# Optimization experiments

Measured on AMD Instinct MI355X. Metric: run time of the kernel, lower is better.

Reference implementation:

```python
import jax, jax.numpy as jnp
import numpy as np
import math

MAX_F, B, D = 512, 32, 1024
H, NUM_OUT = 16, 4
S = D // H  # subspace size = 64
FC_HID = 4096
MASK_VAL = -50.0  # the original writes -50 (not -inf) into padded logits


def setup_inputs() -> dict:
    key = jax.random.key(0)
    k = jax.random.split(key, 7)
    x = jax.random.normal(k[0], (MAX_F, B, D), dtype=jnp.float32)
    num_frames = jax.random.randint(k[1], (B,), 1, MAX_F + 1)
    query = jax.random.normal(k[2], (NUM_OUT, H, S), dtype=jnp.float32)  # attn_query_vecs
    W1 = jax.random.normal(k[3], (D * NUM_OUT, FC_HID), dtype=jnp.float32) * 0.02
    b1 = jnp.zeros((FC_HID,), dtype=jnp.float32)
    W2 = jax.random.normal(k[4], (FC_HID, NUM_OUT), dtype=jnp.float32) * 0.02
    b2 = jnp.zeros((NUM_OUT,), dtype=jnp.float32)
    return {"x": x, "num_frames": num_frames, "query": query,
            "W1": W1, "b1": b1, "W2": W2, "b2": b2}


def reference(x, num_frames, query, W1, b1, W2, b2):
    # x: (F, B, D) padded per-frame features (encoder = identity, pad value irrelevant
    # because we re-mask below, matching pad-with-zeros in the original).
    F, Bz, Dz = x.shape
    O, Hh, Ss = query.shape
    scale = math.sqrt(Ss)
    mask = jnp.arange(F)[:, None] < num_frames[None, :]            # (F, B)
    hq = x.reshape(F, Bz, Hh, Ss)                                  # (F, B, H, S)
    # per-head query-key dot products for all num_out queries at once
    alpha = jnp.einsum('fbhs,ohs->ofbh', hq, query) / scale        # (O, F, B, H)
    alpha = jnp.where(mask[None, :, :, None], alpha, MASK_VAL)
    attn = jax.nn.softmax(alpha, axis=1)                           # softmax over frames
    h_pad = jnp.where(mask[:, :, None, None], hq, 0.0)             # zero-padded features
    h_vid = jnp.einsum('fbhs,ofbh->obhs', h_pad, attn)             # (O, B, H, S)
    # stack(dim=1) then view(B, -1) -> concat num_out feature blocks per sample
    h_cat = jnp.transpose(h_vid, (1, 0, 2, 3)).reshape(Bz, O * Hh * Ss)
    out = jax.nn.relu(h_cat @ W1 + b1) @ W2 + b2                   # (B, num_out)
    return out, attn
```

## Files before the change

kernel.cpp:

```cpp
#include <hip/hip_runtime.h>
#include <math.h>

#define MAXF 512
#define BZ   32
#define DD   1024
#define HH   16
#define OO   4
#define SS   64
#define FCH  4096
#define KPARTS 8

typedef __attribute__((ext_vector_type(8))) short short8;
typedef __attribute__((ext_vector_type(4))) float f32x4;

__device__ inline short f2bf(float f) {
    unsigned u = __float_as_uint(f);
    u += 0x7FFFu + ((u >> 16) & 1u);
    return (short)(u >> 16);
}

__global__ __launch_bounds__(256) void logits_kernel(
    const float* __restrict__ x, const int* __restrict__ num_frames,
    const float* __restrict__ query, float* __restrict__ logits,
    float2* __restrict__ cstats)
{
    __shared__ __align__(16) float tile[64][68];
    __shared__ __align__(16) float sq[OO][64];

    const int tid   = threadIdx.x;
    const int bh    = blockIdx.x >> 3;
    const int fc    = blockIdx.x & 7;
    const int b     = bh >> 4, h = bh & 15;
    const int nf    = num_frames[b];
    const int fbase = fc * 64;
    const bool act  = (fbase < nf);

    const int o = tid >> 6, f = tid & 63;
    sq[o][f] = query[(size_t)(o * HH + h) * SS + f];

    if (act) {
        #pragma unroll
        for (int k = 0; k < 4; ++k) {
            int idx = tid + k * 256;
            int fr = idx >> 4, s4 = (idx & 15) * 4;
            float4 v = *(const float4*)(x + (size_t)(fbase + fr) * (BZ * DD)
                                          + (size_t)b * DD + h * SS + s4);
            *(float4*)&tile[fr][s4] = v;
        }
    }
    __syncthreads();

    float lg = -50.0f;
    if (act) {
        const float4* trow = (const float4*)&tile[f][0];
        const float4* qrow = (const float4*)&sq[o][0];
        float dot = 0.f;
        #pragma unroll
        for (int i = 0; i < 16; ++i) {
            float4 t = trow[i];
            float4 q = qrow[i];
            dot += t.x * q.x + t.y * q.y + t.z * q.z + t.w * q.w;
        }
        if (fbase + f < nf) lg = dot * 0.125f;
    }
    logits[((size_t)bh * OO + o) * MAXF + fbase + f] = lg;

    float mc = lg;
    #pragma unroll
    for (int d = 32; d; d >>= 1) mc = fmaxf(mc, __shfl_xor(mc, d, 64));
    float sc = __expf(lg - mc);
    #pragma unroll
    for (int d = 32; d; d >>= 1) sc += __shfl_xor(sc, d, 64);
    if (f == 0) cstats[(bh * OO + o) * 8 + fc] = make_float2(mc, sc);
}

__global__ __launch_bounds__(256) void wsum_kernel(
    const float* __restrict__ x, const int* __restrict__ num_frames,
    const float* __restrict__ query, const float2* __restrict__ cstats,
    float* __restrict__ hcat)
{
    __shared__ __align__(16) float tile[64][68];
    __shared__ __align__(16) float sq[OO][64];
    __shared__ __align__(16) float attc[OO][64];

    const int tid   = threadIdx.x;
    const int bh    = blockIdx.x >> 3;
    const int fc    = blockIdx.x & 7;
    const int b     = bh >> 4, h = bh & 15;
    const int nf    = num_frames[b];
    const int fbase = fc * 64;
    const bool act  = (fbase < nf);

    if (!act && fc != 0) return;

    const int o = tid >> 6, lane = tid & 63;
    sq[o][lane] = query[(size_t)(o * HH + h) * SS + lane];

    if (act) {
        #pragma unroll
        for (int k = 0; k < 4; ++k) {
            int idx = tid + k * 256;
            int fr = idx >> 4, s4 = (idx & 15) * 4;
            float4 v = *(const float4*)(x + (size_t)(fbase + fr) * (BZ * DD)
                                          + (size_t)b * DD + h * SS + s4);
            *(float4*)&tile[fr][s4] = v;
        }
    }
    __syncthreads();

    const float2* cs = cstats + (bh * OO + o) * 8;
    float m = -1e30f;
    #pragma unroll
    for (int k = 0; k < 8; ++k) m = fmaxf(m, cs[k].x);
    float s = 0.f;
    #pragma unroll
    for (int k = 0; k < 8; ++k) s += cs[k].y * __expf(cs[k].x - m);
    const float inv = 1.0f / s;

    float p = 0.f;
    if (act) {
        const float4* trow = (const float4*)&tile[lane][0];
        const float4* qrow = (const float4*)&sq[o][0];
        float dot = 0.f;
        #pragma unroll
        for (int i = 0; i < 16; ++i) {
            float4 t = trow[i];
            float4 q = qrow[i];
            dot += t.x * q.x + t.y * q.y + t.z * q.z + t.w * q.w;
        }
        if (fbase + lane < nf) p = __expf(dot * 0.125f - m) * inv;
    }
    attc[o][lane] = p;
    __syncthreads();

    float acc = 0.f;
    if (act) {
        const float4* a4 = (const float4*)&attc[o][0];
        #pragma unroll
        for (int i = 0; i < 16; ++i) {
            float4 a = a4[i];
            acc += a.x * tile[i * 4 + 0][lane];
            acc += a.y * tile[i * 4 + 1][lane];
            acc += a.z * tile[i * 4 + 2][lane];
            acc += a.w * tile[i * 4 + 3][lane];
        }
    }
    const float POIS = (fc == 0) ? __uint_as_float(0xAAAAAAAAu) : 0.f;
    atomicAdd(&hcat[(size_t)b * FCH + o * (HH * SS) + h * SS + lane], acc - POIS);
}

__global__ __launch_bounds__(256) void attn_out_kernel(
    const float* __restrict__ logits, const float2* __restrict__ cstats,
    float* __restrict__ attn_out)
{
    __shared__ float tile[64][65];
    __shared__ float sm[64], sv[64];
    const int o     = blockIdx.z;
    const int fbase = blockIdx.x * 64;
    const int gbase = blockIdx.y * 64;
    const int c  = threadIdx.x & 63;
    const int r4 = threadIdx.x >> 6;

    if (threadIdx.x < 64) {
        const float2* cs = cstats + ((gbase + threadIdx.x) * OO + o) * 8;
        float m = -1e30f;
        #pragma unroll
        for (int k = 0; k < 8; ++k) m = fmaxf(m, cs[k].x);
        float s = 0.f;
        #pragma unroll
        for (int k = 0; k < 8; ++k) s += cs[k].y * __expf(cs[k].x - m);
        sm[threadIdx.x] = m;
        sv[threadIdx.x] = 1.0f / s;
    }
    for (int r = r4; r < 64; r += 4)
        tile[r][c] = logits[((size_t)(gbase + r) * OO + o) * MAXF + fbase + c];
    __syncthreads();
    for (int r = r4; r < 64; r += 4)
        attn_out[((size_t)o * MAXF + fbase + r) * (BZ * HH) + gbase + c] =
            __expf(tile[c][r] - sm[c]) * sv[c];
}

__global__ __launch_bounds__(256) void fc1_mfma_kernel(
    const float* __restrict__ hcat, const float* __restrict__ W1,
    float* __restrict__ part)
{
    const int tid  = threadIdx.x;
    const int w    = tid >> 6;
    const int lane = tid & 63;
    const int L15  = lane & 15, q = lane >> 4;
    const int j0   = blockIdx.x * 64 + w * 16;
    const int kp   = blockIdx.y;
    const int k0   = kp * 512;

    f32x4 acc0 = {0.f, 0.f, 0.f, 0.f};
    f32x4 acc1 = {0.f, 0.f, 0.f, 0.f};

    #pragma unroll 2
    for (int s = 0; s < 16; ++s) {
        const int kk = k0 + s * 32 + q * 8;

        const float4* a0p = (const float4*)(hcat + (size_t)L15 * FCH + kk);
        const float4* a1p = (const float4*)(hcat + (size_t)(L15 + 16) * FCH + kk);
        float4 a0l = a0p[0], a0h = a0p[1];
        float4 a1l = a1p[0], a1h = a1p[1];
        short8 af0, af1;
        af0[0]=f2bf(a0l.x); af0[1]=f2bf(a0l.y); af0[2]=f2bf(a0l.z); af0[3]=f2bf(a0l.w);
        af0[4]=f2bf(a0h.x); af0[5]=f2bf(a0h.y); af0[6]=f2bf(a0h.z); af0[7]=f2bf(a0h.w);
        af1[0]=f2bf(a1l.x); af1[1]=f2bf(a1l.y); af1[2]=f2bf(a1l.z); af1[3]=f2bf(a1l.w);
        af1[4]=f2bf(a1h.x); af1[5]=f2bf(a1h.y); af1[6]=f2bf(a1h.z); af1[7]=f2bf(a1h.w);

        const float* bp = W1 + (size_t)kk * FCH + j0 + L15;
        short8 bf;
        bf[0] = f2bf(bp[0 * (size_t)FCH]);
        bf[1] = f2bf(bp[1 * (size_t)FCH]);
        bf[2] = f2bf(bp[2 * (size_t)FCH]);
        bf[3] = f2bf(bp[3 * (size_t)FCH]);
        bf[4] = f2bf(bp[4 * (size_t)FCH]);
        bf[5] = f2bf(bp[5 * (size_t)FCH]);
        bf[6] = f2bf(bp[6 * (size_t)FCH]);
        bf[7] = f2bf(bp[7 * (size_t)FCH]);

        acc0 = __builtin_amdgcn_mfma_f32_16x16x32_bf16(af0, bf, acc0, 0, 0, 0);
        acc1 = __builtin_amdgcn_mfma_f32_16x16x32_bf16(af1, bf, acc1, 0, 0, 0);
    }

    float* pout = part + (size_t)kp * 32 * FCH;
    #pragma unroll
    for (int r = 0; r < 4; ++r) {
        pout[(size_t)(q * 4 + r) * FCH + j0 + L15]        = acc0[r];
        pout[(size_t)(16 + q * 4 + r) * FCH + j0 + L15]   = acc1[r];
    }
}

__global__ __launch_bounds__(256) void fc2_kernel(
    const float* __restrict__ part, const float* __restrict__ b1,
    const float* __restrict__ W2, const float* __restrict__ b2,
    float* __restrict__ out)
{
    __shared__ float red[4][4];
    const int b = blockIdx.x, tid = threadIdx.x;
    float a0 = 0.f, a1 = 0.f, a2 = 0.f, a3 = 0.f;
    #pragma unroll
    for (int k = 0; k < 4; ++k) {
        int j4 = tid + k * 256;
        float4 hv = make_float4(0.f, 0.f, 0.f, 0.f);
        #pragma unroll
        for (int kp = 0; kp < KPARTS; ++kp) {
            float4 pv = ((const float4*)(part + (size_t)(kp * 32 + b) * FCH))[j4];
            hv.x += pv.x; hv.y += pv.y; hv.z += pv.z; hv.w += pv.w;
        }
        float4 bv = ((const float4*)b1)[j4];
        float h0 = fmaxf(hv.x + bv.x, 0.f), h1 = fmaxf(hv.y + bv.y, 0.f);
        float h2 = fmaxf(hv.z + bv.z, 0.f), h3 = fmaxf(hv.w + bv.w, 0.f);
        float4 w0 = ((const float4*)W2)[j4 * 4 + 0];
        float4 w1 = ((const float4*)W2)[j4 * 4 + 1];
        float4 w2 = ((const float4*)W2)[j4 * 4 + 2];
        float4 w3 = ((const float4*)W2)[j4 * 4 + 3];
        a0 += h0 * w0.x + h1 * w1.x + h2 * w2.x + h3 * w3.x;
        a1 += h0 * w0.y + h1 * w1.y + h2 * w2.y + h3 * w3.y;
        a2 += h0 * w0.z + h1 * w1.z + h2 * w2.z + h3 * w3.z;
        a3 += h0 * w0.w + h1 * w1.w + h2 * w2.w + h3 * w3.w;
    }
    #pragma unroll
    for (int d = 32; d; d >>= 1) {
        a0 += __shfl_xor(a0, d, 64);
        a1 += __shfl_xor(a1, d, 64);
        a2 += __shfl_xor(a2, d, 64);
        a3 += __shfl_xor(a3, d, 64);
    }
    const int wv = tid >> 6, lane = tid & 63;
    if (lane == 0) { red[wv][0] = a0; red[wv][1] = a1; red[wv][2] = a2; red[wv][3] = a3; }
    __syncthreads();
    if (tid < 4) {
        float s = red[0][tid] + red[1][tid] + red[2][tid] + red[3][tid] + b2[tid];
        out[b * OO + tid] = s;
    }
}

extern "C" void kernel_launch(void* const* d_in, const int* in_sizes, int n_in,
                              void* d_out, int out_size, void* d_ws, size_t ws_size,
                              hipStream_t stream)
{
    const float* x          = (const float*)d_in[0];
    const int*   num_frames = (const int*)  d_in[1];
    const float* query      = (const float*)d_in[2];
    const float* W1         = (const float*)d_in[3];
    const float* b1         = (const float*)d_in[4];
    const float* W2         = (const float*)d_in[5];
    const float* b2         = (const float*)d_in[6];

    float* out      = (float*)d_out;
    float* attn_out = out + BZ * OO;

    float*  ws        = (float*)d_ws;
    float*  ws_logits = ws;
    float2* ws_cstats = (float2*)(ws + 1048576);
    float*  ws_hcat   = ws + 1048576 + 32768;
    float*  ws_part   = ws_logits;

    logits_kernel  <<<4096, 256, 0, stream>>>(x, num_frames, query, ws_logits, ws_cstats);
    wsum_kernel    <<<4096, 256, 0, stream>>>(x, num_frames, query, ws_cstats, ws_hcat);
    attn_out_kernel<<<dim3(8, 8, 4), 256, 0, stream>>>(ws_logits, ws_cstats, attn_out);
    fc1_mfma_kernel<<<dim3(64, KPARTS), 256, 0, stream>>>(ws_hcat, W1, ws_part);
    fc2_kernel     <<<BZ, 256, 0, stream>>>(ws_part, b1, W2, b2, out);
}
```

Measured before the change: 190.8 us.

## Fuse logits and weighted-sum into single-pass online-softmax attention kernel

```diff
diff --git a/kernel.cpp b/kernel.cpp
--- a/kernel.cpp
+++ b/kernel.cpp
@@ -19,138 +19,188 @@
     return (short)(u >> 16);
 }
 
-__global__ __launch_bounds__(256) void logits_kernel(
+#define MUL4(A,S)  do{ (A).x*=(S); (A).y*=(S); (A).z*=(S); (A).w*=(S); }while(0)
+#define FMA4(A,P,V) do{ (A).x += (P)*(V).x; (A).y += (P)*(V).y; \
+                        (A).z += (P)*(V).z; (A).w += (P)*(V).w; }while(0)
+#define RSUMF(F) do{ F += __shfl_xor(F,4,64); F += __shfl_xor(F,8,64); \
+                     F += __shfl_xor(F,16,64); F += __shfl_xor(F,32,64); }while(0)
+#define RMAXF(F) do{ F = fmaxf(F,__shfl_xor(F,4,64)); F = fmaxf(F,__shfl_xor(F,8,64)); \
+                     F = fmaxf(F,__shfl_xor(F,16,64)); F = fmaxf(F,__shfl_xor(F,32,64)); }while(0)
+#define BFLY4(A) do{ RSUMF((A).x); RSUMF((A).y); RSUMF((A).z); RSUMF((A).w); }while(0)
+#define CCOMP(V,C) ((C)==0?(V).x:(C)==1?(V).y:(C)==2?(V).z:(V).w)
+#define GETJ(V0,V1,V2,V3,J) ((J)<4?CCOMP(V0,(J)&3):(J)<8?CCOMP(V1,(J)&3): \
+                             (J)<12?CCOMP(V2,(J)&3):CCOMP(V3,(J)&3))
+#define DOT16(R,QA,QB,QC,QD) \
+    R = xa0.x*(QA).x + xa0.y*(QA).y + xa0.z*(QA).z + xa0.w*(QA).w \
+      + xa1.x*(QB).x + xa1.y*(QB).y + xa1.z*(QB).z + xa1.w*(QB).w \
+      + xa2.x*(QC).x + xa2.y*(QC).y + xa2.z*(QC).z + xa2.w*(QC).w \
+      + xa3.x*(QD).x + xa3.y*(QD).y + xa3.z*(QD).z + xa3.w*(QD).w
+#define SCALE_ACC() do{ \
+    MUL4(a00,sc0);MUL4(a01,sc0);MUL4(a02,sc0);MUL4(a03,sc0); \
+    MUL4(a10,sc1);MUL4(a11,sc1);MUL4(a12,sc1);MUL4(a13,sc1); \
+    MUL4(a20,sc2);MUL4(a21,sc2);MUL4(a22,sc2);MUL4(a23,sc2); \
+    MUL4(a30,sc3);MUL4(a31,sc3);MUL4(a32,sc3);MUL4(a33,sc3); }while(0)
+
+__global__ __launch_bounds__(256) void attn_fused_kernel(
     const float* __restrict__ x, const int* __restrict__ num_frames,
     const float* __restrict__ query, float* __restrict__ logits,
-    float2* __restrict__ cstats)
-{
-    __shared__ __align__(16) float tile[64][68];
-    __shared__ __align__(16) float sq[OO][64];
-
-    const int tid   = threadIdx.x;
-    const int bh    = blockIdx.x >> 3;
-    const int fc    = blockIdx.x & 7;
-    const int b     = bh >> 4, h = bh & 15;
-    const int nf    = num_frames[b];
-    const int fbase = fc * 64;
-    const bool act  = (fbase < nf);
-
-    const int o = tid >> 6, f = tid & 63;
-    sq[o][f] = query[(size_t)(o * HH + h) * SS + f];
-
-    if (act) {
+    float2* __restrict__ fstats, float* __restrict__ hcat)
+{
+    __shared__ __align__(16) float sq[OO][SS];
+    __shared__ float wmS[4][OO], wsS[4][OO];
+    __shared__ __align__(16) float accsh[4][4][16][OO];
+
+    const int tid  = threadIdx.x;
+    const int bh   = blockIdx.x;
+    const int b    = bh >> 4, h = bh & 15;
+    const int nf   = num_frames[b];
+    const int w    = tid >> 6;
+    const int lane = tid & 63;
+    const int sg   = tid & 3;
+    const int fch  = tid >> 2;
+
+    sq[w][lane] = query[(size_t)(w * HH + h) * SS + lane];
+    __syncthreads();
+
+    float4 q00,q01,q02,q03,q10,q11,q12,q13,q20,q21,q22,q23,q30,q31,q32,q33;
+    {
+        const float4* q0 = (const float4*)&sq[0][0];
+        q00=q0[sg]; q01=q0[sg+4]; q02=q0[sg+8]; q03=q0[sg+12];
+        const float4* q1 = (const float4*)&sq[1][0];
+        q10=q1[sg]; q11=q1[sg+4]; q12=q1[sg+8]; q13=q1[sg+12];
+        const float4* q2 = (const float4*)&sq[2][0];
+        q20=q2[sg]; q21=q2[sg+4]; q22=q2[sg+8]; q23=q2[sg+12];
+        const float4* q3 = (const float4*)&sq[3][0];
+        q30=q3[sg]; q31=q3[sg+4]; q32=q3[sg+8]; q33=q3[sg+12];
+    }
+
+    const float* xbase = x + (size_t)b * DD + (size_t)h * SS;
+
+    float m0=-1e30f,m1=-1e30f,m2=-1e30f,m3=-1e30f;
+    float s0=0.f,s1=0.f,s2=0.f,s3=0.f;
+    float4 a00={0,0,0,0},a01={0,0,0,0},a02={0,0,0,0},a03={0,0,0,0};
+    float4 a10={0,0,0,0},a11={0,0,0,0},a12={0,0,0,0},a13={0,0,0,0};
+    float4 a20={0,0,0,0},a21={0,0,0,0},a22={0,0,0,0},a23={0,0,0,0};
+    float4 a30={0,0,0,0},a31={0,0,0,0},a32={0,0,0,0},a33={0,0,0,0};
+
+    float4 xa0,xa1,xa2,xa3;
+    {
+        const float4* p = (const float4*)(xbase + (size_t)fch * (BZ*DD));
+        xa0=p[sg]; xa1=p[sg+4]; xa2=p[sg+8]; xa3=p[sg+12];
+    }
+
+    #pragma unroll
+    for (int fc = 0; fc < 8; ++fc) {
+        const int fbase = fc * 64;
+        const bool act  = (fbase < nf);
+        float4 xb0={0,0,0,0},xb1={0,0,0,0},xb2={0,0,0,0},xb3={0,0,0,0};
+        const bool actn = (fc < 7) && (fbase + 64 < nf);
+        if (actn) {
+            const float4* p = (const float4*)(xbase + (size_t)(fbase + 64 + fch) * (BZ*DD));
+            xb0=p[sg]; xb1=p[sg+4]; xb2=p[sg+8]; xb3=p[sg+12];
+        }
+        if (act) {
+            float d0,d1,d2,d3;
+            DOT16(d0,q00,q01,q02,q03);
+            DOT16(d1,q10,q11,q12,q13);
+            DOT16(d2,q20,q21,q22,q23);
+            DOT16(d3,q30,q31,q32,q33);
+            d0 += __shfl_xor(d0,1,64); d0 += __shfl_xor(d0,2,64);
+            d1 += __shfl_xor(d1,1,64); d1 += __shfl_xor(d1,2,64);
+            d2 += __shfl_xor(d2,1,64); d2 += __shfl_xor(d2,2,64);
+            d3 += __shfl_xor(d3,1,64); d3 += __shfl_xor(d3,2,64);
+            const bool valid = (fbase + fch) < nf;
+            float lg0 = valid ? d0 * 0.125f : -50.f;
+            float lg1 = valid ? d1 * 0.125f : -50.f;
+            float lg2 = valid ? d2 * 0.125f : -50.f;
+            float lg3 = valid ? d3 * 0.125f : -50.f;
+            float c0=lg0,c1=lg1,c2=lg2,c3=lg3;
+            RMAXF(c0); RMAXF(c1); RMAXF(c2); RMAXF(c3);
+            float n0=fmaxf(m0,c0), n1=fmaxf(m1,c1), n2=fmaxf(m2,c2), n3=fmaxf(m3,c3);
+            float e0=__expf(lg0-n0), e1=__expf(lg1-n1), e2=__expf(lg2-n2), e3=__expf(lg3-n3);
+            float t0=e0,t1=e1,t2=e2,t3=e3;
+            RSUMF(t0); RSUMF(t1); RSUMF(t2); RSUMF(t3);
+            float sc0=__expf(m0-n0), sc1=__expf(m1-n1), sc2=__expf(m2-n2), sc3=__expf(m3-n3);
+            s0 = s0*sc0 + t0; s1 = s1*sc1 + t1; s2 = s2*sc2 + t2; s3 = s3*sc3 + t3;
+            m0=n0; m1=n1; m2=n2; m3=n3;
+            if (sc0<1.f || sc1<1.f || sc2<1.f || sc3<1.f) SCALE_ACC();
+            float p0 = valid ? e0 : 0.f;
+            float p1 = valid ? e1 : 0.f;
+            float p2 = valid ? e2 : 0.f;
+            float p3 = valid ? e3 : 0.f;
+            FMA4(a00,p0,xa0); FMA4(a01,p0,xa1); FMA4(a02,p0,xa2); FMA4(a03,p0,xa3);
+            FMA4(a10,p1,xa0); FMA4(a11,p1,xa1); FMA4(a12,p1,xa2); FMA4(a13,p1,xa3);
+            FMA4(a20,p2,xa0); FMA4(a21,p2,xa1); FMA4(a22,p2,xa2); FMA4(a23,p2,xa3);
+            FMA4(a30,p3,xa0); FMA4(a31,p3,xa1); FMA4(a32,p3,xa2); FMA4(a33,p3,xa3);
+            float lgw = sg==0?lg0 : sg==1?lg1 : sg==2?lg2 : lg3;
+            logits[((size_t)bh*OO + sg)*MAXF + fbase + fch] = lgw;
+        } else {
+            float n0=fmaxf(m0,-50.f), n1=fmaxf(m1,-50.f), n2=fmaxf(m2,-50.f), n3=fmaxf(m3,-50.f);
+            float sc0=__expf(m0-n0), sc1=__expf(m1-n1), sc2=__expf(m2-n2), sc3=__expf(m3-n3);
+            s0 = s0*sc0 + 16.f*__expf(-50.f-n0);
+            s1 = s1*sc1 + 16.f*__expf(-50.f-n1);
+            s2 = s2*sc2 + 16.f*__expf(-50.f-n2);
+            s3 = s3*sc3 + 16.f*__expf(-50.f-n3);
+            if (sc0<1.f || sc1<1.f || sc2<1.f || sc3<1.f) SCALE_ACC();
+            m0=n0; m1=n1; m2=n2; m3=n3;
+            logits[((size_t)bh*OO + sg)*MAXF + fbase + fch] = -50.f;
+        }
+        xa0=xb0; xa1=xb1; xa2=xb2; xa3=xb3;
+    }
+
+    if (lane == 0) {
+        wmS[w][0]=m0; wmS[w][1]=m1; wmS[w][2]=m2; wmS[w][3]=m3;
+        wsS[w][0]=s0; wsS[w][1]=s1; wsS[w][2]=s2; wsS[w][3]=s3;
+    }
+    __syncthreads();
+    float gm0 = fmaxf(fmaxf(wmS[0][0],wmS[1][0]), fmaxf(wmS[2][0],wmS[3][0]));
+    float gm1 = fmaxf(fmaxf(wmS[0][1],wmS[1][1]), fmaxf(wmS[2][1],wmS[3][1]));
+    float gm2 = fmaxf(fmaxf(wmS[0][2],wmS[1][2]), fmaxf(wmS[2][2],wmS[3][2]));
+    float gm3 = fmaxf(fmaxf(wmS[0][3],wmS[1][3]), fmaxf(wmS[2][3],wmS[3][3]));
+    float gs0 = wsS[0][0]*__expf(wmS[0][0]-gm0) + wsS[1][0]*__expf(wmS[1][0]-gm0)
+              + wsS[2][0]*__expf(wmS[2][0]-gm0) + wsS[3][0]*__expf(wmS[3][0]-gm0);
+    float gs1 = wsS[0][1]*__expf(wmS[0][1]-gm1) + wsS[1][1]*__expf(wmS[1][1]-gm1)
+              + wsS[2][1]*__expf(wmS[2][1]-gm1) + wsS[3][1]*__expf(wmS[3][1]-gm1);
+    float gs2 = wsS[0][2]*__expf(wmS[0][2]-gm2) + wsS[1][2]*__expf(wmS[1][2]-gm2)
+              + wsS[2][2]*__expf(wmS[2][2]-gm2) + wsS[3][2]*__expf(wmS[3][2]-gm2);
+    float gs3 = wsS[0][3]*__expf(wmS[0][3]-gm3) + wsS[1][3]*__expf(wmS[1][3]-gm3)
+              + wsS[2][3]*__expf(wmS[2][3]-gm3) + wsS[3][3]*__expf(wmS[3][3]-gm3);
+    float scl0=__expf(m0-gm0), scl1=__expf(m1-gm1), scl2=__expf(m2-gm2), scl3=__expf(m3-gm3);
+
+    BFLY4(a00); BFLY4(a01); BFLY4(a02); BFLY4(a03);
+    BFLY4(a10); BFLY4(a11); BFLY4(a12); BFLY4(a13);
+    BFLY4(a20); BFLY4(a21); BFLY4(a22); BFLY4(a23);
+    BFLY4(a30); BFLY4(a31); BFLY4(a32); BFLY4(a33);
+
+    if ((lane >> 2) == 0) {
         #pragma unroll
-        for (int k = 0; k < 4; ++k) {
-            int idx = tid + k * 256;
-            int fr = idx >> 4, s4 = (idx & 15) * 4;
-            float4 v = *(const float4*)(x + (size_t)(fbase + fr) * (BZ * DD)
-                                          + (size_t)b * DD + h * SS + s4);
-            *(float4*)&tile[fr][s4] = v;
+        for (int j = 0; j < 16; ++j) {
+            float v0 = GETJ(a00,a01,a02,a03,j) * scl0;
+            float v1 = GETJ(a10,a11,a12,a13,j) * scl1;
+            float v2 = GETJ(a20,a21,a22,a23,j) * scl2;
+            float v3 = GETJ(a30,a31,a32,a33,j) * scl3;
+            *(float4*)&accsh[w][sg][j][0] = make_float4(v0,v1,v2,v3);
         }
     }
     __syncthreads();
-
-    float lg = -50.0f;
-    if (act) {
-        const float4* trow = (const float4*)&tile[f][0];
-        const float4* qrow = (const float4*)&sq[o][0];
-        float dot = 0.f;
-        #pragma unroll
-        for (int i = 0; i < 16; ++i) {
-            float4 t = trow[i];
-            float4 q = qrow[i];
-            dot += t.x * q.x + t.y * q.y + t.z * q.z + t.w * q.w;
-        }
-        if (fbase + f < nf) lg = dot * 0.125f;
-    }
-    logits[((size_t)bh * OO + o) * MAXF + fbase + f] = lg;
-
-    float mc = lg;
-    #pragma unroll
-    for (int d = 32; d; d >>= 1) mc = fmaxf(mc, __shfl_xor(mc, d, 64));
-    float sc = __expf(lg - mc);
-    #pragma unroll
-    for (int d = 32; d; d >>= 1) sc += __shfl_xor(sc, d, 64);
-    if (f == 0) cstats[(bh * OO + o) * 8 + fc] = make_float2(mc, sc);
-}
-
-__global__ __launch_bounds__(256) void wsum_kernel(
-    const float* __restrict__ x, const int* __restrict__ num_frames,
-    const float* __restrict__ query, const float2* __restrict__ cstats,
-    float* __restrict__ hcat)
-{
-    __shared__ __align__(16) float tile[64][68];
-    __shared__ __align__(16) float sq[OO][64];
-    __shared__ __align__(16) float attc[OO][64];
-
-    const int tid   = threadIdx.x;
-    const int bh    = blockIdx.x >> 3;
-    const int fc    = blockIdx.x & 7;
-    const int b     = bh >> 4, h = bh & 15;
-    const int nf    = num_frames[b];
-    const int fbase = fc * 64;
-    const bool act  = (fbase < nf);
-
-    if (!act && fc != 0) return;
-
-    const int o = tid >> 6, lane = tid & 63;
-    sq[o][lane] = query[(size_t)(o * HH + h) * SS + lane];
-
-    if (act) {
-        #pragma unroll
-        for (int k = 0; k < 4; ++k) {
-            int idx = tid + k * 256;
-            int fr = idx >> 4, s4 = (idx & 15) * 4;
-            float4 v = *(const float4*)(x + (size_t)(fbase + fr) * (BZ * DD)
-                                          + (size_t)b * DD + h * SS + s4);
-            *(float4*)&tile[fr][s4] = v;
-        }
-    }
-    __syncthreads();
-
-    const float2* cs = cstats + (bh * OO + o) * 8;
-    float m = -1e30f;
-    #pragma unroll
-    for (int k = 0; k < 8; ++k) m = fmaxf(m, cs[k].x);
-    float s = 0.f;
-    #pragma unroll
-    for (int k = 0; k < 8; ++k) s += cs[k].y * __expf(cs[k].x - m);
-    const float inv = 1.0f / s;
-
-    float p = 0.f;
-    if (act) {
-        const float4* trow = (const float4*)&tile[lane][0];
-        const float4* qrow = (const float4*)&sq[o][0];
-        float dot = 0.f;
-        #pragma unroll
-        for (int i = 0; i < 16; ++i) {
-            float4 t = trow[i];
-            float4 q = qrow[i];
-            dot += t.x * q.x + t.y * q.y + t.z * q.z + t.w * q.w;
-        }
-        if (fbase + lane < nf) p = __expf(dot * 0.125f - m) * inv;
-    }
-    attc[o][lane] = p;
-    __syncthreads();
-
-    float acc = 0.f;
-    if (act) {
-        const float4* a4 = (const float4*)&attc[o][0];
-        #pragma unroll
-        for (int i = 0; i < 16; ++i) {
-            float4 a = a4[i];
-            acc += a.x * tile[i * 4 + 0][lane];
-            acc += a.y * tile[i * 4 + 1][lane];
-            acc += a.z * tile[i * 4 + 2][lane];
-            acc += a.w * tile[i * 4 + 3][lane];
-        }
-    }
-    const float POIS = (fc == 0) ? __uint_as_float(0xAAAAAAAAu) : 0.f;
-    atomicAdd(&hcat[(size_t)b * FCH + o * (HH * SS) + h * SS + lane], acc - POIS);
+    {
+        const int oo = tid >> 6, s = tid & 63;
+        const int ssg = (s >> 2) & 3, sj = ((s >> 4) << 2) | (s & 3);
+        float v = accsh[0][ssg][sj][oo] + accsh[1][ssg][sj][oo]
+                + accsh[2][ssg][sj][oo] + accsh[3][ssg][sj][oo];
+        float gso = oo==0?gs0 : oo==1?gs1 : oo==2?gs2 : gs3;
+        hcat[(size_t)b*FCH + (size_t)oo*(HH*SS) + h*SS + s] = v * (1.0f/gso);
+    }
+    if (tid == 0) {
+        fstats[bh*OO+0] = make_float2(gm0, 1.0f/gs0);
+        fstats[bh*OO+1] = make_float2(gm1, 1.0f/gs1);
+        fstats[bh*OO+2] = make_float2(gm2, 1.0f/gs2);
+        fstats[bh*OO+3] = make_float2(gm3, 1.0f/gs3);
+    }
 }
 
 __global__ __launch_bounds__(256) void attn_out_kernel(
-    const float* __restrict__ logits, const float2* __restrict__ cstats,
+    const float* __restrict__ logits, const float2* __restrict__ fstats,
     float* __restrict__ attn_out)
 {
     __shared__ float tile[64][65];
@@ -162,15 +212,9 @@
     const int r4 = threadIdx.x >> 6;
 
     if (threadIdx.x < 64) {
-        const float2* cs = cstats + ((gbase + threadIdx.x) * OO + o) * 8;
-        float m = -1e30f;
-        #pragma unroll
-        for (int k = 0; k < 8; ++k) m = fmaxf(m, cs[k].x);
-        float s = 0.f;
-        #pragma unroll
-        for (int k = 0; k < 8; ++k) s += cs[k].y * __expf(cs[k].x - m);
-        sm[threadIdx.x] = m;
-        sv[threadIdx.x] = 1.0f / s;
+        float2 st = fstats[(gbase + threadIdx.x) * OO + o];
+        sm[threadIdx.x] = st.x;
+        sv[threadIdx.x] = st.y;
     }
     for (int r = r4; r < 64; r += 4)
         tile[r][c] = logits[((size_t)(gbase + r) * OO + o) * MAXF + fbase + c];
@@ -294,13 +338,13 @@
 
     float*  ws        = (float*)d_ws;
     float*  ws_logits = ws;
-    float2* ws_cstats = (float2*)(ws + 1048576);
-    float*  ws_hcat   = ws + 1048576 + 32768;
+    float2* ws_fstats = (float2*)(ws + 1048576);
+    float*  ws_hcat   = ws + 1048576 + 4096;
     float*  ws_part   = ws_logits;
 
-    logits_kernel  <<<4096, 256, 0, stream>>>(x, num_frames, query, ws_logits, ws_cstats);
-    wsum_kernel    <<<4096, 256, 0, stream>>>(x, num_frames, query, ws_cstats, ws_hcat);
-    attn_out_kernel<<<dim3(8, 8, 4), 256, 0, stream>>>(ws_logits, ws_cstats, attn_out);
+    attn_fused_kernel<<<BZ * HH, 256, 0, stream>>>(x, num_frames, query,
+                                                   ws_logits, ws_fstats, ws_hcat);
+    attn_out_kernel<<<dim3(8, 8, 4), 256, 0, stream>>>(ws_logits, ws_fstats, attn_out);
     fc1_mfma_kernel<<<dim3(64, KPARTS), 256, 0, stream>>>(ws_hcat, W1, ws_part);
     fc2_kernel     <<<BZ, 256, 0, stream>>>(ws_part, b1, W2, b2, out);
 }
```

After: 192.7 us. Within noise of the previous version (+1.0%).
